# Kernel tuning notes

Hardware: AMD Instinct MI355X
Metric: run time of the kernel (lower is better)

The kernel has to match this reference:

```python
import jax, jax.numpy as jnp
from jax import lax
import numpy as np

C = 256       # residual_channels == skip_channels
B = 4
T = 4096
LATENT = 128
NB = 4        # n_blocks
NL = 10       # n_layers
ENC_DILS = tuple(2 ** i for i in range(NL)) * NB   # 40 encoder blocks
DEC_DILS = tuple(2 ** i for i in range(NL))        # 10 decoder blocks


def causal_conv(x, W, b, d):
    # x: [B, Cin, T], W: [Cout, Cin, k], left-pad by (k-1)*d for causality
    pad = (W.shape[-1] - 1) * d
    y = lax.conv_general_dilated(x, W, (1,), [(pad, 0)], rhs_dilation=(d,),
                                 dimension_numbers=('NCH', 'OIH', 'NCH'))
    return y + b[None, :, None]


def gated_block(h, Wf, bf, Wg, bg, Wr, br, Ws, bs, d):
    f = jnp.tanh(causal_conv(h, Wf, bf, d))
    g = jax.nn.sigmoid(causal_conv(h, Wg, bg, d))
    out = f * g
    res = jnp.einsum('oc,bct->bot', Wr, out) + br[None, :, None] + h
    skip = jnp.einsum('oc,bct->bot', Ws, out) + bs[None, :, None]
    return res, skip


def setup_inputs() -> dict:
    key = jax.random.key(0)
    ks = jax.random.split(key, 24)
    s = 0.05
    nE = NB * NL
    d = {}
    d['x'] = jax.random.normal(ks[0], (B, 1, T), jnp.float32)
    d['eps'] = jax.random.normal(ks[1], (B, LATENT), jnp.float32)
    d['enc_in_W'] = jax.random.normal(ks[2], (C, 1, 2)) * s
    d['enc_in_b'] = jnp.zeros((C,), jnp.float32)
    d['enc_Wf'] = jax.random.normal(ks[3], (nE, C, C, 2)) * s
    d['enc_bf'] = jnp.zeros((nE, C), jnp.float32)
    d['enc_Wg'] = jax.random.normal(ks[4], (nE, C, C, 2)) * s
    d['enc_bg'] = jnp.zeros((nE, C), jnp.float32)
    d['enc_Wr'] = jax.random.normal(ks[5], (nE, C, C)) * s
    d['enc_br'] = jnp.zeros((nE, C), jnp.float32)
    d['enc_Ws'] = jax.random.normal(ks[6], (nE, C, C)) * s
    d['enc_bs'] = jnp.zeros((nE, C), jnp.float32)
    d['fc_mu_W'] = jax.random.normal(ks[7], (LATENT, C)) * s
    d['fc_mu_b'] = jnp.zeros((LATENT,), jnp.float32)
    d['fc_lv_W'] = jax.random.normal(ks[8], (LATENT, C)) * s
    d['fc_lv_b'] = jnp.zeros((LATENT,), jnp.float32)
    d['dec_in_W'] = jax.random.normal(ks[9], (C, LATENT)) * s
    d['dec_in_b'] = jnp.zeros((C,), jnp.float32)
    d['dec_Wf'] = jax.random.normal(ks[10], (NL, C, C, 2)) * s
    d['dec_bf'] = jnp.zeros((NL, C), jnp.float32)
    d['dec_Wg'] = jax.random.normal(ks[11], (NL, C, C, 2)) * s
    d['dec_bg'] = jnp.zeros((NL, C), jnp.float32)
    d['dec_Wr'] = jax.random.normal(ks[12], (NL, C, C)) * s
    d['dec_br'] = jnp.zeros((NL, C), jnp.float32)
    d['out_W'] = jax.random.normal(ks[13], (1, C)) * s
    d['out_b'] = jnp.zeros((1,), jnp.float32)
    return d


def _forward(x, eps, enc_in_W, enc_in_b, enc_Wf, enc_bf, enc_Wg, enc_bg,
             enc_Wr, enc_br, enc_Ws, enc_bs, fc_mu_W, fc_mu_b, fc_lv_W, fc_lv_b,
             dec_in_W, dec_in_b, dec_Wf, dec_bf, dec_Wg, dec_bg, dec_Wr, dec_br,
             out_W, out_b):
    # --- encode ---
    h = causal_conv(x, enc_in_W, enc_in_b, 1)
    skip_sum = jnp.zeros((h.shape[0], C, h.shape[2]), h.dtype)
    for i, dil in enumerate(ENC_DILS):
        h, skip = gated_block(h, enc_Wf[i], enc_bf[i], enc_Wg[i], enc_bg[i],
                              enc_Wr[i], enc_br[i], enc_Ws[i], enc_bs[i], dil)
        skip_sum = skip_sum + skip
    pooled = skip_sum.mean(axis=-1)                      # [B, C]
    mu = pooled @ fc_mu_W.T + fc_mu_b                    # [B, LATENT]
    logvar = pooled @ fc_lv_W.T + fc_lv_b
    # --- reparameterize ---
    z = mu + eps * jnp.exp(0.5 * logvar)
    # --- decode (length-1 sequence) ---
    h2 = (jnp.einsum('ol,bl->bo', dec_in_W, z) + dec_in_b)[:, :, None]  # [B, C, 1]
    for i, dil in enumerate(DEC_DILS):
        f = jnp.tanh(causal_conv(h2, dec_Wf[i], dec_bf[i], dil))
        g = jax.nn.sigmoid(causal_conv(h2, dec_Wg[i], dec_bg[i], dil))
        out = f * g
        h2 = jnp.einsum('oc,bct->bot', dec_Wr[i], out) + dec_br[i][None, :, None] + h2
    y = jnp.einsum('oc,bct->bot', out_W, h2) + out_b[None, :, None]     # [B, 1, 1]
    return (y, mu, logvar)


def reference(x, eps, enc_in_W, enc_in_b, enc_Wf, enc_bf, enc_Wg, enc_bg,
              enc_Wr, enc_br, enc_Ws, enc_bs, fc_mu_W, fc_mu_b, fc_lv_W, fc_lv_b,
              dec_in_W, dec_in_b, dec_Wf, dec_bf, dec_Wg, dec_bg, dec_Wr, dec_br,
              out_W, out_b):
    return _forward(x, eps, enc_in_W, enc_in_b, enc_Wf, enc_bf, enc_Wg, enc_bg,
                    enc_Wr, enc_br, enc_Ws, enc_bs, fc_mu_W, fc_mu_b, fc_lv_W, fc_lv_b,
                    dec_in_W, dec_in_b, dec_Wf, dec_bf, dec_Wg, dec_bg, dec_Wr, dec_br,
                    out_W, out_b)
```

## Files before the change

kernel.cpp:

```cpp
#include <hip/hip_runtime.h>

typedef unsigned short u16;
typedef __attribute__((ext_vector_type(8))) __bf16 bf16x8;
typedef __attribute__((ext_vector_type(4))) float f32x4;

constexpr int C = 256;
constexpr int T = 4096;
constexpr int B = 4;
constexpr int NENC = 40;
constexpr int NDEC = 10;
constexpr int TILE = 64;

__device__ __forceinline__ float bf2f(u16 v) {
  union { unsigned u; float f; } x;
  x.u = ((unsigned)v) << 16;
  return x.f;
}
__device__ __forceinline__ u16 f2bf(float f) {
  union { float ff; unsigned u; } x;
  x.ff = f;
  unsigned r = x.u + 0x7fffu + ((x.u >> 16) & 1u);
  return (u16)(r >> 16);
}
__device__ __forceinline__ int swz(int row, int col) {
  int g = ((row & 7) ^ (row >> 3)) & 7;
  return row * 512 + (col ^ (g << 3));
}

typedef __attribute__((address_space(1))) const unsigned int* gp1_t;
typedef __attribute__((address_space(3))) unsigned int* lp3_t;
__device__ __forceinline__ void gl_lds16(const u16* g, u16* l) {
  __builtin_amdgcn_global_load_lds((gp1_t)(const void*)g, (lp3_t)(void*)l, 16, 0, 0);
}

__global__ void k_pack1(const float* __restrict__ Wf, const float* __restrict__ Wg,
                        u16* __restrict__ penc1, int total) {
  int p = blockIdx.x * 256 + threadIdx.x;
  if (p >= total) return;
  int lane = p & 63;
  int s = (p >> 6) & 3;
  int c = (p >> 8) & 15;
  int wv = (p >> 12) & 7;
  int layer = p >> 15;
  int co = wv * 32 + (s & 1) * 16 + (lane & 15);
  int k = c * 32 + (lane >> 4) * 8;
  const float* src = (s >= 2 ? Wg : Wf) + ((size_t)layer * C + co) * 512 + k;
  u16* dst = penc1 + (size_t)p * 8;
#pragma unroll
  for (int r = 0; r < 8; ++r) dst[r] = f2bf(src[r]);
}

__global__ void k_pack2(const float* __restrict__ Wr, u16* __restrict__ penc2, int total) {
  int p = blockIdx.x * 256 + threadIdx.x;
  if (p >= total) return;
  int lane = p & 63;
  int s = (p >> 6) & 1;
  int c = (p >> 7) & 7;
  int wv = (p >> 10) & 7;
  int layer = p >> 13;
  int co = wv * 32 + s * 16 + (lane & 15);
  int k = c * 32 + (lane >> 4) * 8;
  const float* src = Wr + ((size_t)layer * C + co) * 256 + k;
  u16* dst = penc2 + (size_t)p * 8;
#pragma unroll
  for (int r = 0; r < 8; ++r) dst[r] = f2bf(src[r]);
}

__global__ void k_packd(const float* __restrict__ dWf, const float* __restrict__ dWg,
                        const float* __restrict__ dWr, const float* __restrict__ dinW,
                        u16* __restrict__ pdfg, u16* __restrict__ pdr,
                        u16* __restrict__ tdin) {
  int p = blockIdx.x * 256 + threadIdx.x;
  if (p < 163840) {
    int lane = p & 63;
    int s = (p >> 6) & 1;
    int c = (p >> 7) & 7;
    int wv = (p >> 10) & 15;
    int layer = p >> 14;
    int co = wv * 16 + (lane & 15);
    int k = c * 32 + (lane >> 4) * 8;
    const float* src = (s ? dWg : dWf) + (((size_t)(layer * C + co)) * C + k) * 2 + 1;
    u16* dst = pdfg + (size_t)p * 8;
#pragma unroll
    for (int r = 0; r < 8; ++r) dst[r] = f2bf(src[2 * r]);
  } else if (p < 245760) {
    int q = p - 163840;
    int lane = q & 63;
    int c = (q >> 6) & 7;
    int wv = (q >> 9) & 15;
    int layer = q >> 13;
    int co = wv * 16 + (lane & 15);
    int k = c * 32 + (lane >> 4) * 8;
    const float* src = dWr + ((size_t)(layer * C + co)) * C + k;
    u16* dst = pdr + (size_t)q * 8;
#pragma unroll
    for (int r = 0; r < 8; ++r) dst[r] = f2bf(src[r]);
  } else if (p < 249856) {
    int u = p - 245760;
#pragma unroll
    for (int r = 0; r < 8; ++r) tdin[u * 8 + r] = f2bf(dinW[u * 8 + r]);
  }
}

__global__ void k_zero(float* __restrict__ p, int n) {
  int i = blockIdx.x * 256 + threadIdx.x;
  if (i < n) p[i] = 0.f;
}

__global__ void k_input(const float* __restrict__ x, const float* __restrict__ W,
                        const float* __restrict__ bin, float* __restrict__ h) {
  int idx = blockIdx.x * 256 + threadIdx.x;
  int t = idx & (T - 1);
  int c = (idx >> 12) & (C - 1);
  int b = idx >> 20;
  float xv = x[b * T + t];
  float xp = (t > 0) ? x[b * T + t - 1] : 0.f;
  h[idx] = W[2 * c] * xp + W[2 * c + 1] * xv + bin[c];
}

__global__ __launch_bounds__(512, 2) void k_enc(
    const float* __restrict__ hin, float* __restrict__ hout, float* __restrict__ rowsum_l,
    const u16* __restrict__ pw1, const float* __restrict__ bfb,
    const float* __restrict__ bgb,
    const u16* __restrict__ pw2, const float* __restrict__ brb,
    int dil) {
  extern __shared__ __align__(16) u16 smem[];
  u16* wb = smem + 64 * 512;
  const int tid = threadIdx.x;
  const int wave = tid >> 6;
  const int lane = tid & 63;
  const int ncol = lane & 15;
  const int quad = lane >> 4;
  const int wg = blockIdx.x;
  const int b = wg >> 6;
  const int t0 = (wg & 63) * TILE;
  const float* hb = hin + b * C * T;

  const int co0 = wave * 32;
  const int kq = quad * 8;
  const int off1 = (wg >> 3) & 15;
  const int off2 = (wg >> 3) & 7;
  const u16* b1 = pw1 + wave * 32768 + lane * 8;
  const u16* b2 = pw2 + wave * 8192 + lane * 8;
  u16* wreg0 = wb + wave * 2048;
  u16* wreg1 = wb + 16384 + wave * 2048;
  const int aoff = lane * 8;

#pragma unroll
  for (int cc = 0; cc < 2; ++cc) {
    u16* ld = cc ? wreg1 : wreg0;
    const u16* gs = b1 + ((off1 + cc) & 15) * 2048;
    gl_lds16(gs, ld);
    gl_lds16(gs + 512, ld + 512);
    gl_lds16(gs + 1024, ld + 1024);
    gl_lds16(gs + 1536, ld + 1536);
  }

  const int n4 = tid & 15;
  const int cib = tid >> 4;
  float4 v[16];
  const bool al4 = ((dil & 3) == 0);
  if (t0 >= dil) {
#pragma unroll
    for (int it2 = 0; it2 < 16; ++it2) {
      int ci = (cib + it2 * 32) & 255;
      int tap = it2 >> 3;
      int tb = t0 + n4 * 4 - (tap ? 0 : dil);
      const float* p = hb + ci * T + tb;
      if (tap || al4) {
        v[it2] = *(const float4*)p;
      } else {
        v[it2].x = p[0]; v[it2].y = p[1]; v[it2].z = p[2]; v[it2].w = p[3];
      }
    }
  } else {
#pragma unroll
    for (int it2 = 0; it2 < 16; ++it2) {
      int ci = (cib + it2 * 32) & 255;
      int tap = it2 >> 3;
      int tb = t0 + n4 * 4 - (tap ? 0 : dil);
      const float* p = hb + ci * T + tb;
      if (tap) {
        v[it2] = *(const float4*)p;
      } else {
        v[it2].x = (tb + 0 >= 0) ? p[0] : 0.f;
        v[it2].y = (tb + 1 >= 0) ? p[1] : 0.f;
        v[it2].z = (tb + 2 >= 0) ? p[2] : 0.f;
        v[it2].w = (tb + 3 >= 0) ? p[3] : 0.f;
      }
    }
  }
#pragma unroll
  for (int it2 = 0; it2 < 8; ++it2) {
    int ci = (cib + it2 * 32) & 255;
    const float* p0 = (const float*)&v[it2];
    const float* p1 = (const float*)&v[it2 + 8];
#pragma unroll
    for (int r = 0; r < 4; ++r) {
      unsigned w32 = (unsigned)f2bf(p0[r]) | ((unsigned)f2bf(p1[r]) << 16);
      *(unsigned*)(&smem[swz(n4 * 4 + r, 2 * ci)]) = w32;
    }
  }
  __syncthreads();

  f32x4 acc[4][4];
#pragma unroll
  for (int m = 0; m < 4; ++m)
#pragma unroll
    for (int nt = 0; nt < 4; ++nt)
      acc[m][nt] = (f32x4){0.f, 0.f, 0.f, 0.f};

#pragma unroll
  for (int c = 0; c < 16; ++c) {
    if (c < 15) asm volatile("s_waitcnt vmcnt(4)" ::: "memory");
    else        asm volatile("s_waitcnt vmcnt(0)" ::: "memory");
    const u16* wr_ = (c & 1) ? wreg1 : wreg0;
    bf16x8 af0 = *(const bf16x8*)(wr_ + aoff);
    bf16x8 af1 = *(const bf16x8*)(wr_ + 512 + aoff);
    bf16x8 af2 = *(const bf16x8*)(wr_ + 1024 + aoff);
    bf16x8 af3 = *(const bf16x8*)(wr_ + 1536 + aoff);
    const int kk = ((c + off1) & 15) * 32 + kq;
    bf16x8 bfr[4];
#pragma unroll
    for (int nt = 0; nt < 4; ++nt)
      bfr[nt] = *(const bf16x8*)(&smem[swz(nt * 16 + ncol, kk)]);
#pragma unroll
    for (int nt = 0; nt < 4; ++nt) {
      acc[0][nt] = __builtin_amdgcn_mfma_f32_16x16x32_bf16(af0, bfr[nt], acc[0][nt], 0, 0, 0);
      acc[1][nt] = __builtin_amdgcn_mfma_f32_16x16x32_bf16(af1, bfr[nt], acc[1][nt], 0, 0, 0);
      acc[2][nt] = __builtin_amdgcn_mfma_f32_16x16x32_bf16(af2, bfr[nt], acc[2][nt], 0, 0, 0);
      acc[3][nt] = __builtin_amdgcn_mfma_f32_16x16x32_bf16(af3, bfr[nt], acc[3][nt], 0, 0, 0);
    }
    if (c + 2 < 16) {
      asm volatile("s_waitcnt lgkmcnt(0)" ::: "memory");
      u16* ld = (c & 1) ? wreg1 : wreg0;
      const u16* gs = b1 + ((c + 2 + off1) & 15) * 2048;
      gl_lds16(gs, ld);
      gl_lds16(gs + 512, ld + 512);
      gl_lds16(gs + 1024, ld + 1024);
      gl_lds16(gs + 1536, ld + 1536);
    }
  }

#pragma unroll
  for (int cc = 0; cc < 2; ++cc) {
    u16* ld = cc ? wreg1 : wreg0;
    const u16* gs = b2 + ((off2 + cc) & 7) * 1024;
    gl_lds16(gs, ld);
    gl_lds16(gs + 512, ld + 512);
  }
  __syncthreads();

  float* rsb = rowsum_l + b * C;
#pragma unroll
  for (int j = 0; j < 2; ++j) {
    const int cob = co0 + j * 16 + quad * 4;
    float bfv[4], bgv[4], rs[4];
#pragma unroll
    for (int r = 0; r < 4; ++r) {
      bfv[r] = bfb[cob + r];
      bgv[r] = bgb[cob + r];
      rs[r] = 0.f;
    }
#pragma unroll
    for (int nt = 0; nt < 4; ++nt) {
      const int n = nt * 16 + ncol;
      u16 pk[4];
#pragma unroll
      for (int r = 0; r < 4; ++r) {
        float fv = acc[j][nt][r] + bfv[r];
        float gv = acc[2 + j][nt][r] + bgv[r];
        float th = 1.f - 2.f / (__expf(2.f * fv) + 1.f);
        float sg = 1.f / (1.f + __expf(-gv));
        float o = th * sg;
        rs[r] += o;
        pk[r] = f2bf(o);
      }
      uint2 w;
      w.x = (unsigned)pk[0] | ((unsigned)pk[1] << 16);
      w.y = (unsigned)pk[2] | ((unsigned)pk[3] << 16);
      *(uint2*)(&smem[swz(n, cob)]) = w;
    }
#pragma unroll
    for (int r = 0; r < 4; ++r) {
      float s = rs[r];
      s += __shfl_xor(s, 1);
      s += __shfl_xor(s, 2);
      s += __shfl_xor(s, 4);
      s += __shfl_xor(s, 8);
      if (ncol == 0) atomicAdd(&rsb[cob + r], s);
    }
  }
  __syncthreads();

  f32x4 acc2[2][4];
#pragma unroll
  for (int m = 0; m < 2; ++m)
#pragma unroll
    for (int nt = 0; nt < 4; ++nt)
      acc2[m][nt] = (f32x4){0.f, 0.f, 0.f, 0.f};

#pragma unroll
  for (int c = 0; c < 8; ++c) {
    if (c < 7) asm volatile("s_waitcnt vmcnt(2)" ::: "memory");
    else       asm volatile("s_waitcnt vmcnt(0)" ::: "memory");
    const u16* wr_ = (c & 1) ? wreg1 : wreg0;
    bf16x8 af0 = *(const bf16x8*)(wr_ + aoff);
    bf16x8 af1 = *(const bf16x8*)(wr_ + 512 + aoff);
    const int kk = ((c + off2) & 7) * 32 + kq;
    bf16x8 bfr[4];
#pragma unroll
    for (int nt = 0; nt < 4; ++nt)
      bfr[nt] = *(const bf16x8*)(&smem[swz(nt * 16 + ncol, kk)]);
#pragma unroll
    for (int nt = 0; nt < 4; ++nt) {
      acc2[0][nt] = __builtin_amdgcn_mfma_f32_16x16x32_bf16(af0, bfr[nt], acc2[0][nt], 0, 0, 0);
      acc2[1][nt] = __builtin_amdgcn_mfma_f32_16x16x32_bf16(af1, bfr[nt], acc2[1][nt], 0, 0, 0);
    }
    if (c + 2 < 8) {
      asm volatile("s_waitcnt lgkmcnt(0)" ::: "memory");
      u16* ld = (c & 1) ? wreg1 : wreg0;
      const u16* gs = b2 + ((c + 2 + off2) & 7) * 1024;
      gl_lds16(gs, ld);
      gl_lds16(gs + 512, ld + 512);
    }
  }
  __syncthreads();

  float* fb = (float*)smem;
#pragma unroll
  for (int m = 0; m < 2; ++m) {
    const int cob = co0 + m * 16 + quad * 4;
#pragma unroll
    for (int nt = 0; nt < 4; ++nt) {
      const int t = nt * 16 + ncol;
#pragma unroll
      for (int r = 0; r < 4; ++r)
        fb[(cob + r) * 66 + t] = acc2[m][nt][r] + brb[cob + r];
    }
  }
  __syncthreads();
  float* ho = hout + b * C * T;
#pragma unroll
  for (int it2 = 0; it2 < 8; ++it2) {
    const int ci = cib + it2 * 32;
    const float* fr = fb + ci * 66 + n4 * 4;
    float4 o;
    o.x = fr[0] + v[it2 + 8].x;
    o.y = fr[1] + v[it2 + 8].y;
    o.z = fr[2] + v[it2 + 8].z;
    o.w = fr[3] + v[it2 + 8].w;
    *(float4*)(ho + ci * T + t0 + n4 * 4) = o;
  }
}

__global__ __launch_bounds__(256) void k_skip(
    const float* __restrict__ encWs, const float* __restrict__ encbs,
    const float* __restrict__ rowsum, float* __restrict__ pooled) {
  __shared__ float rs[B][C];
  const int l = blockIdx.x;
  const int co = threadIdx.x;
  for (int i = co; i < B * C; i += 256) rs[i >> 8][i & 255] = rowsum[l * B * C + i];
  __syncthreads();
  const float* Wrow = encWs + (size_t)l * C * C + co * C;
  float bs = encbs[l * C + co] * (float)T;
  float d[B] = {0.f, 0.f, 0.f, 0.f};
  for (int ci = 0; ci < C; ci += 4) {
    float4 w = *(const float4*)(Wrow + ci);
#pragma unroll
    for (int b = 0; b < B; ++b)
      d[b] += w.x * rs[b][ci] + w.y * rs[b][ci + 1] + w.z * rs[b][ci + 2] + w.w * rs[b][ci + 3];
  }
#pragma unroll
  for (int b = 0; b < B; ++b) atomicAdd(&pooled[b * C + co], d[b] + bs);
}

__global__ __launch_bounds__(256) void k_fc(
    const float* __restrict__ pooled,
    const float* __restrict__ muW, const float* __restrict__ mub,
    const float* __restrict__ lvW, const float* __restrict__ lvb,
    float* __restrict__ mlbuf, float* __restrict__ dout) {
  __shared__ float pm[B * C];
  const int tid = threadIdx.x;
  for (int i = tid; i < B * C; i += 256) pm[i] = pooled[i] * (1.f / (float)T);
  __syncthreads();
  const int waveG = blockIdx.x * 4 + (tid >> 6);
  const int lane = tid & 63;
  for (int j = 0; j < 16; ++j) {
    int d = waveG * 16 + j;
    int b = d >> 8, r = d & 255, which = r >> 7, l = r & 127;
    const float* Wrow = (which ? lvW : muW) + l * C;
    const float* p = pm + b * C;
    float s = Wrow[lane] * p[lane] + Wrow[lane + 64] * p[lane + 64] +
              Wrow[lane + 128] * p[lane + 128] + Wrow[lane + 192] * p[lane + 192];
#pragma unroll
    for (int off = 32; off; off >>= 1) s += __shfl_xor(s, off);
    if (lane == 0) {
      float val = s + (which ? lvb[l] : mub[l]);
      mlbuf[which * 512 + b * 128 + l] = val;
      dout[4 + which * 512 + b * 128 + l] = val;
    }
  }
}

__global__ __launch_bounds__(1024, 1) void k_dec(
    const float* __restrict__ mlbuf, const float* __restrict__ eps,
    const u16* __restrict__ tdin, const float* __restrict__ dinb,
    const u16* __restrict__ pdfg, const float* __restrict__ dbf,
    const float* __restrict__ dbg,
    const u16* __restrict__ pdr, const float* __restrict__ dbr,
    const float* __restrict__ outW, const float* __restrict__ outb,
    float* __restrict__ dout) {
  extern __shared__ __align__(16) u16 dsm[];
  __shared__ __align__(16) u16 Ah[16][264];
  __shared__ __align__(16) u16 Ao[16][264];
  __shared__ float h2f[4][256];
  __shared__ float outred[4];
  const int tid = threadIdx.x;
  const int wave = tid >> 6;
  const int lane = tid & 63;
  const int ncol = lane & 15;
  const int quad = lane >> 4;
  const int kq = quad * 8;
  const int co = wave * 16 + ncol;
  u16* wreg = dsm + wave * 4096;

  bf16x8 tdw[4];
  {
    const u16* wp = tdin + co * 128;
#pragma unroll
    for (int it = 0; it < 4; ++it) tdw[it] = *(const bf16x8*)(wp + it * 32 + kq);
  }

  if (tid < 512) {
    int b = tid >> 7, l = tid & 127;
    float mu = mlbuf[b * 128 + l];
    float lv = mlbuf[512 + b * 128 + l];
    Ah[b][l] = f2bf(mu + eps[b * 128 + l] * expf(0.5f * lv));
  }
  if (tid < 4) outred[tid] = 0.f;
  __syncthreads();

  {
    f32x4 acch = (f32x4){0.f, 0.f, 0.f, 0.f};
#pragma unroll
    for (int it = 0; it < 4; ++it) {
      bf16x8 af = *(const bf16x8*)(&Ah[ncol][it * 32 + kq]);
      acch = __builtin_amdgcn_mfma_f32_16x16x32_bf16(af, tdw[it], acch, 0, 0, 0);
    }
    __syncthreads();
    if (quad == 0) {
      float bias = dinb[co];
#pragma unroll
      for (int r = 0; r < 4; ++r) {
        float hv = acch[r] + bias;
        h2f[r][co] = hv;
        Ah[r][co] = f2bf(hv);
      }
    }
  }
  {
    const u16* fb = pdfg + wave * 8192 + lane * 8;
#pragma unroll
    for (int cc = 0; cc < 4; ++cc) {
      gl_lds16(fb + cc * 1024, wreg + cc * 1024);
      gl_lds16(fb + cc * 1024 + 512, wreg + cc * 1024 + 512);
    }
  }
  __syncthreads();

  for (int i = 0; i < NDEC; ++i) {
    const u16* fb = pdfg + (i * 16 + wave) * 8192 + lane * 8;
    const u16* rb = pdr + (i * 16 + wave) * 4096 + lane * 8;

    f32x4 accf = (f32x4){0.f, 0.f, 0.f, 0.f};
    f32x4 accg = (f32x4){0.f, 0.f, 0.f, 0.f};
#pragma unroll
    for (int c = 0; c < 8; ++c) {
      if (c == 4) asm volatile("s_waitcnt vmcnt(6)" ::: "memory");
      else if (c == 5) asm volatile("s_waitcnt vmcnt(4)" ::: "memory");
      else if (c == 6) asm volatile("s_waitcnt vmcnt(2)" ::: "memory");
      else if (c == 7) asm volatile("s_waitcnt vmcnt(0)" ::: "memory");
      const u16* bufp = wreg + (c & 3) * 1024;
      bf16x8 bf_ = *(const bf16x8*)(bufp + lane * 8);
      bf16x8 bg_ = *(const bf16x8*)(bufp + 512 + lane * 8);
      bf16x8 af = *(const bf16x8*)(&Ah[ncol][c * 32 + kq]);
      accf = __builtin_amdgcn_mfma_f32_16x16x32_bf16(af, bf_, accf, 0, 0, 0);
      accg = __builtin_amdgcn_mfma_f32_16x16x32_bf16(af, bg_, accg, 0, 0, 0);
      if (c < 4) {
        asm volatile("s_waitcnt lgkmcnt(0)" ::: "memory");
        gl_lds16(fb + (c + 4) * 1024, wreg + (c & 3) * 1024);
        gl_lds16(fb + (c + 4) * 1024 + 512, wreg + (c & 3) * 1024 + 512);
      }
    }
    asm volatile("s_waitcnt lgkmcnt(0)" ::: "memory");
#pragma unroll
    for (int cc = 0; cc < 4; ++cc) gl_lds16(rb + cc * 512, wreg + cc * 1024);

    if (quad == 0) {
      float bfv = dbf[i * C + co];
      float bgv = dbg[i * C + co];
#pragma unroll
      for (int r = 0; r < 4; ++r) {
        float fv = accf[r] + bfv;
        float gv = accg[r] + bgv;
        float th = 1.f - 2.f / (__expf(2.f * fv) + 1.f);
        float sg = 1.f / (1.f + __expf(-gv));
        Ao[r][co] = f2bf(th * sg);
      }
    }
    __syncthreads();

    f32x4 accr = (f32x4){0.f, 0.f, 0.f, 0.f};
#pragma unroll
    for (int c = 0; c < 8; ++c) {
      if (c == 4) asm volatile("s_waitcnt vmcnt(3)" ::: "memory");
      else if (c == 5) asm volatile("s_waitcnt vmcnt(2)" ::: "memory");
      else if (c == 6) asm volatile("s_waitcnt vmcnt(1)" ::: "memory");
      else if (c == 7) asm volatile("s_waitcnt vmcnt(0)" ::: "memory");
      bf16x8 br_ = *(const bf16x8*)(wreg + (c & 3) * 1024 + lane * 8);
      bf16x8 af = *(const bf16x8*)(&Ao[ncol][c * 32 + kq]);
      accr = __builtin_amdgcn_mfma_f32_16x16x32_bf16(af, br_, accr, 0, 0, 0);
      if (c < 4) {
        asm volatile("s_waitcnt lgkmcnt(0)" ::: "memory");
        gl_lds16(rb + (c + 4) * 512, wreg + (c & 3) * 1024);
      }
    }
    if (i + 1 < NDEC) {
      const u16* nfb = pdfg + ((i + 1) * 16 + wave) * 8192 + lane * 8;
      asm volatile("s_waitcnt lgkmcnt(0)" ::: "memory");
#pragma unroll
      for (int cc = 0; cc < 4; ++cc) {
        gl_lds16(nfb + cc * 1024, wreg + cc * 1024);
        gl_lds16(nfb + cc * 1024 + 512, wreg + cc * 1024 + 512);
      }
    }
    if (quad == 0) {
      float brv = dbr[i * C + co];
#pragma unroll
      for (int r = 0; r < 4; ++r) {
        float hv = h2f[r][co] + accr[r] + brv;
        h2f[r][co] = hv;
        Ah[r][co] = f2bf(hv);
      }
    }
    __syncthreads();
  }

  {
    int b = tid >> 8, c = tid & 255;
    float val = outW[c] * h2f[b][c];
#pragma unroll
    for (int off = 32; off; off >>= 1) val += __shfl_xor(val, off);
    if (lane == 0) atomicAdd(&outred[b], val);
  }
  __syncthreads();
  if (tid < 4) dout[tid] = outred[tid] + outb[0];
}

extern "C" void kernel_launch(void* const* d_in, const int* in_sizes, int n_in,
                              void* d_out, int out_size, void* d_ws, size_t ws_size,
                              hipStream_t stream) {
  const float* x      = (const float*)d_in[0];
  const float* eps    = (const float*)d_in[1];
  const float* encinW = (const float*)d_in[2];
  const float* encinb = (const float*)d_in[3];
  const float* encWf  = (const float*)d_in[4];
  const float* encbf  = (const float*)d_in[5];
  const float* encWg  = (const float*)d_in[6];
  const float* encbg  = (const float*)d_in[7];
  const float* encWr  = (const float*)d_in[8];
  const float* encbr  = (const float*)d_in[9];
  const float* encWs  = (const float*)d_in[10];
  const float* encbs  = (const float*)d_in[11];
  const float* muW    = (const float*)d_in[12];
  const float* mub    = (const float*)d_in[13];
  const float* lvW    = (const float*)d_in[14];
  const float* lvb    = (const float*)d_in[15];
  const float* dinW   = (const float*)d_in[16];
  const float* dinb   = (const float*)d_in[17];
  const float* dWf    = (const float*)d_in[18];
  const float* dbf    = (const float*)d_in[19];
  const float* dWg    = (const float*)d_in[20];
  const float* dbg    = (const float*)d_in[21];
  const float* dWr    = (const float*)d_in[22];
  const float* dbr    = (const float*)d_in[23];
  const float* outW   = (const float*)d_in[24];
  const float* outb   = (const float*)d_in[25];
  float* dout = (float*)d_out;

  char* ws = (char*)d_ws;
  float* hA = (float*)ws;
  float* hB = hA + (size_t)B * C * T;
  float* pooled = hB + (size_t)B * C * T;
  float* mlbuf = pooled + B * C;
  float* rowsum = mlbuf + 1024;
  u16* penc1 = (u16*)(rowsum + NENC * B * C);
  u16* penc2 = penc1 + (size_t)10485760;
  u16* pdfg = penc2 + (size_t)2621440;
  u16* pdr = pdfg + (size_t)1310720;
  u16* tdin = pdr + (size_t)655360;

  (void)hipFuncSetAttribute(reinterpret_cast<const void*>(k_enc),
                            hipFuncAttributeMaxDynamicSharedMemorySize, 131072);
  (void)hipFuncSetAttribute(reinterpret_cast<const void*>(k_dec),
                            hipFuncAttributeMaxDynamicSharedMemorySize, 131072);

  k_pack1<<<(1310720 + 255) / 256, 256, 0, stream>>>(encWf, encWg, penc1, 1310720);
  k_pack2<<<(327680 + 255) / 256, 256, 0, stream>>>(encWr, penc2, 327680);
  k_packd<<<(249856 + 255) / 256, 256, 0, stream>>>(dWf, dWg, dWr, dinW, pdfg, pdr, tdin);

  const int nZ = B * C + 1024 + NENC * B * C;
  k_zero<<<(nZ + 255) / 256, 256, 0, stream>>>(pooled, nZ);
  k_input<<<(B * C * T) / 256, 256, 0, stream>>>(x, encinW, encinb, hA);

  for (int i = 0; i < NENC; ++i) {
    const int dil = 1 << (i % 10);
    const float* hi = (i & 1) ? hB : hA;
    float* ho = (i & 1) ? hA : hB;
    k_enc<<<256, 512, 131072, stream>>>(
        hi, ho, rowsum + (size_t)i * B * C,
        penc1 + (size_t)i * 262144, encbf + (size_t)i * C,
        encbg + (size_t)i * C,
        penc2 + (size_t)i * 65536, encbr + (size_t)i * C,
        dil);
  }

  k_skip<<<NENC, 256, 0, stream>>>(encWs, encbs, rowsum, pooled);
  k_fc<<<16, 256, 0, stream>>>(pooled, muW, mub, lvW, lvb, mlbuf, dout);
  k_dec<<<1, 1024, 131072, stream>>>(mlbuf, eps, tdin, dinb, pdfg, dbf, dbg,
                                     pdr, dbr, outW, outb, dout);
}
```

Baseline: 1.287 ms.

## Fuse 40 encoder launches into a persistent kernel with per-tile dataflow flags

The 40 per-layer encoder launches become one persistent kernel that loops over layers inside each workgroup. Per-(layer, batch, tile) flags in workspace replace kernel boundaries. Before reading its input, a workgroup spins until the previous layer's needed neighbouring tiles, including those that still read the buffer it will overwrite, have published their results. This removes launch gaps and whole-grid barriers between layers so fast tiles can move ahead. The cost is spin-wait overhead, and it depends on all 256 workgroups being resident at once.

```diff
diff --git a/kernel.cpp b/kernel.cpp
--- a/kernel.cpp
+++ b/kernel.cpp
@@ -118,12 +118,12 @@
   h[idx] = W[2 * c] * xp + W[2 * c + 1] * xv + bin[c];
 }
 
-__global__ __launch_bounds__(512, 2) void k_enc(
-    const float* __restrict__ hin, float* __restrict__ hout, float* __restrict__ rowsum_l,
-    const u16* __restrict__ pw1, const float* __restrict__ bfb,
-    const float* __restrict__ bgb,
-    const u16* __restrict__ pw2, const float* __restrict__ brb,
-    int dil) {
+__global__ __launch_bounds__(512, 2) void k_encp(
+    float* __restrict__ hA, float* __restrict__ hB, float* __restrict__ rowsum,
+    const u16* __restrict__ penc1, const float* __restrict__ encbf,
+    const float* __restrict__ encbg,
+    const u16* __restrict__ penc2, const float* __restrict__ encbr,
+    int* __restrict__ flags) {
   extern __shared__ __align__(16) u16 smem[];
   u16* wb = smem + 64 * 512;
   const int tid = threadIdx.x;
@@ -133,224 +133,258 @@
   const int quad = lane >> 4;
   const int wg = blockIdx.x;
   const int b = wg >> 6;
-  const int t0 = (wg & 63) * TILE;
-  const float* hb = hin + b * C * T;
+  const int tile = wg & 63;
+  const int t0 = tile * TILE;
 
   const int co0 = wave * 32;
   const int kq = quad * 8;
   const int off1 = (wg >> 3) & 15;
   const int off2 = (wg >> 3) & 7;
-  const u16* b1 = pw1 + wave * 32768 + lane * 8;
-  const u16* b2 = pw2 + wave * 8192 + lane * 8;
+  const int n4 = tid & 15;
+  const int cib = tid >> 4;
+  const int aoff = lane * 8;
   u16* wreg0 = wb + wave * 2048;
   u16* wreg1 = wb + 16384 + wave * 2048;
-  const int aoff = lane * 8;
-
-#pragma unroll
-  for (int cc = 0; cc < 2; ++cc) {
-    u16* ld = cc ? wreg1 : wreg0;
-    const u16* gs = b1 + ((off1 + cc) & 15) * 2048;
-    gl_lds16(gs, ld);
-    gl_lds16(gs + 512, ld + 512);
-    gl_lds16(gs + 1024, ld + 1024);
-    gl_lds16(gs + 1536, ld + 1536);
-  }
-
-  const int n4 = tid & 15;
-  const int cib = tid >> 4;
-  float4 v[16];
-  const bool al4 = ((dil & 3) == 0);
-  if (t0 >= dil) {
-#pragma unroll
-    for (int it2 = 0; it2 < 16; ++it2) {
-      int ci = (cib + it2 * 32) & 255;
-      int tap = it2 >> 3;
-      int tb = t0 + n4 * 4 - (tap ? 0 : dil);
-      const float* p = hb + ci * T + tb;
-      if (tap || al4) {
-        v[it2] = *(const float4*)p;
-      } else {
-        v[it2].x = p[0]; v[it2].y = p[1]; v[it2].z = p[2]; v[it2].w = p[3];
-      }
-    }
-  } else {
-#pragma unroll
-    for (int it2 = 0; it2 < 16; ++it2) {
-      int ci = (cib + it2 * 32) & 255;
-      int tap = it2 >> 3;
-      int tb = t0 + n4 * 4 - (tap ? 0 : dil);
-      const float* p = hb + ci * T + tb;
-      if (tap) {
-        v[it2] = *(const float4*)p;
-      } else {
-        v[it2].x = (tb + 0 >= 0) ? p[0] : 0.f;
-        v[it2].y = (tb + 1 >= 0) ? p[1] : 0.f;
-        v[it2].z = (tb + 2 >= 0) ? p[2] : 0.f;
-        v[it2].w = (tb + 3 >= 0) ? p[3] : 0.f;
-      }
-    }
-  }
-#pragma unroll
-  for (int it2 = 0; it2 < 8; ++it2) {
-    int ci = (cib + it2 * 32) & 255;
-    const float* p0 = (const float*)&v[it2];
-    const float* p1 = (const float*)&v[it2 + 8];
-#pragma unroll
-    for (int r = 0; r < 4; ++r) {
-      unsigned w32 = (unsigned)f2bf(p0[r]) | ((unsigned)f2bf(p1[r]) << 16);
-      *(unsigned*)(&smem[swz(n4 * 4 + r, 2 * ci)]) = w32;
-    }
-  }
-  __syncthreads();
-
-  f32x4 acc[4][4];
-#pragma unroll
-  for (int m = 0; m < 4; ++m)
-#pragma unroll
-    for (int nt = 0; nt < 4; ++nt)
-      acc[m][nt] = (f32x4){0.f, 0.f, 0.f, 0.f};
-
-#pragma unroll
-  for (int c = 0; c < 16; ++c) {
-    if (c < 15) asm volatile("s_waitcnt vmcnt(4)" ::: "memory");
-    else        asm volatile("s_waitcnt vmcnt(0)" ::: "memory");
-    const u16* wr_ = (c & 1) ? wreg1 : wreg0;
-    bf16x8 af0 = *(const bf16x8*)(wr_ + aoff);
-    bf16x8 af1 = *(const bf16x8*)(wr_ + 512 + aoff);
-    bf16x8 af2 = *(const bf16x8*)(wr_ + 1024 + aoff);
-    bf16x8 af3 = *(const bf16x8*)(wr_ + 1536 + aoff);
-    const int kk = ((c + off1) & 15) * 32 + kq;
-    bf16x8 bfr[4];
-#pragma unroll
-    for (int nt = 0; nt < 4; ++nt)
-      bfr[nt] = *(const bf16x8*)(&smem[swz(nt * 16 + ncol, kk)]);
-#pragma unroll
-    for (int nt = 0; nt < 4; ++nt) {
-      acc[0][nt] = __builtin_amdgcn_mfma_f32_16x16x32_bf16(af0, bfr[nt], acc[0][nt], 0, 0, 0);
-      acc[1][nt] = __builtin_amdgcn_mfma_f32_16x16x32_bf16(af1, bfr[nt], acc[1][nt], 0, 0, 0);
-      acc[2][nt] = __builtin_amdgcn_mfma_f32_16x16x32_bf16(af2, bfr[nt], acc[2][nt], 0, 0, 0);
-      acc[3][nt] = __builtin_amdgcn_mfma_f32_16x16x32_bf16(af3, bfr[nt], acc[3][nt], 0, 0, 0);
-    }
-    if (c + 2 < 16) {
-      asm volatile("s_waitcnt lgkmcnt(0)" ::: "memory");
-      u16* ld = (c & 1) ? wreg1 : wreg0;
-      const u16* gs = b1 + ((c + 2 + off1) & 15) * 2048;
+
+  for (int i = 0; i < NENC; ++i) {
+    const int dil = 1 << (i % 10);
+    const float* hi = (i & 1) ? hB : hA;
+    float* ho = (i & 1) ? hA : hB;
+    const float* hb = hi + b * C * T;
+    const u16* b1 = penc1 + (size_t)i * 262144 + wave * 32768 + lane * 8;
+    const u16* b2 = penc2 + (size_t)i * 65536 + wave * 8192 + lane * 8;
+    const float* bfb = encbf + i * C;
+    const float* bgb = encbg + i * C;
+    const float* brb = encbr + i * C;
+
+#pragma unroll
+    for (int cc = 0; cc < 2; ++cc) {
+      u16* ld = cc ? wreg1 : wreg0;
+      const u16* gs = b1 + ((off1 + cc) & 15) * 2048;
       gl_lds16(gs, ld);
       gl_lds16(gs + 512, ld + 512);
       gl_lds16(gs + 1024, ld + 1024);
       gl_lds16(gs + 1536, ld + 1536);
     }
-  }
-
-#pragma unroll
-  for (int cc = 0; cc < 2; ++cc) {
-    u16* ld = cc ? wreg1 : wreg0;
-    const u16* gs = b2 + ((off2 + cc) & 7) * 1024;
-    gl_lds16(gs, ld);
-    gl_lds16(gs + 512, ld + 512);
-  }
-  __syncthreads();
-
-  float* rsb = rowsum_l + b * C;
-#pragma unroll
-  for (int j = 0; j < 2; ++j) {
-    const int cob = co0 + j * 16 + quad * 4;
-    float bfv[4], bgv[4], rs[4];
-#pragma unroll
-    for (int r = 0; r < 4; ++r) {
-      bfv[r] = bfb[cob + r];
-      bgv[r] = bgb[cob + r];
-      rs[r] = 0.f;
-    }
-#pragma unroll
-    for (int nt = 0; nt < 4; ++nt) {
-      const int n = nt * 16 + ncol;
-      u16 pk[4];
+
+    if (i > 0) {
+      const int dprev = 1 << ((i - 1) % 10);
+      int lo = t0 - dil;
+      lo = (lo < 0) ? 0 : (lo >> 6);
+      int hiT = tile + ((dprev + 63) >> 6);
+      if (hiT > 63) hiT = 63;
+      if (wave == 0) {
+        const int n = hiT - lo + 1;
+        if (lane < n) {
+          const int* fp = flags + ((i - 1) * 4 + b) * 64 + lo + lane;
+          while (__hip_atomic_load(fp, __ATOMIC_ACQUIRE, __HIP_MEMORY_SCOPE_AGENT) == 0)
+            __builtin_amdgcn_s_sleep(2);
+        }
+      }
+      __syncthreads();
+    }
+
+    float4 v[16];
+    const bool al4 = ((dil & 3) == 0);
+    if (t0 >= dil) {
+#pragma unroll
+      for (int it2 = 0; it2 < 16; ++it2) {
+        int ci = (cib + it2 * 32) & 255;
+        int tap = it2 >> 3;
+        int tb = t0 + n4 * 4 - (tap ? 0 : dil);
+        const float* p = hb + ci * T + tb;
+        if (tap || al4) {
+          v[it2] = *(const float4*)p;
+        } else {
+          v[it2].x = p[0]; v[it2].y = p[1]; v[it2].z = p[2]; v[it2].w = p[3];
+        }
+      }
+    } else {
+#pragma unroll
+      for (int it2 = 0; it2 < 16; ++it2) {
+        int ci = (cib + it2 * 32) & 255;
+        int tap = it2 >> 3;
+        int tb = t0 + n4 * 4 - (tap ? 0 : dil);
+        const float* p = hb + ci * T + tb;
+        if (tap) {
+          v[it2] = *(const float4*)p;
+        } else {
+          v[it2].x = (tb + 0 >= 0) ? p[0] : 0.f;
+          v[it2].y = (tb + 1 >= 0) ? p[1] : 0.f;
+          v[it2].z = (tb + 2 >= 0) ? p[2] : 0.f;
+          v[it2].w = (tb + 3 >= 0) ? p[3] : 0.f;
+        }
+      }
+    }
+#pragma unroll
+    for (int it2 = 0; it2 < 8; ++it2) {
+      int ci = (cib + it2 * 32) & 255;
+      const float* p0 = (const float*)&v[it2];
+      const float* p1 = (const float*)&v[it2 + 8];
 #pragma unroll
       for (int r = 0; r < 4; ++r) {
-        float fv = acc[j][nt][r] + bfv[r];
-        float gv = acc[2 + j][nt][r] + bgv[r];
-        float th = 1.f - 2.f / (__expf(2.f * fv) + 1.f);
-        float sg = 1.f / (1.f + __expf(-gv));
-        float o = th * sg;
-        rs[r] += o;
-        pk[r] = f2bf(o);
-      }
-      uint2 w;
-      w.x = (unsigned)pk[0] | ((unsigned)pk[1] << 16);
-      w.y = (unsigned)pk[2] | ((unsigned)pk[3] << 16);
-      *(uint2*)(&smem[swz(n, cob)]) = w;
-    }
-#pragma unroll
-    for (int r = 0; r < 4; ++r) {
-      float s = rs[r];
-      s += __shfl_xor(s, 1);
-      s += __shfl_xor(s, 2);
-      s += __shfl_xor(s, 4);
-      s += __shfl_xor(s, 8);
-      if (ncol == 0) atomicAdd(&rsb[cob + r], s);
-    }
-  }
-  __syncthreads();
-
-  f32x4 acc2[2][4];
-#pragma unroll
-  for (int m = 0; m < 2; ++m)
-#pragma unroll
-    for (int nt = 0; nt < 4; ++nt)
-      acc2[m][nt] = (f32x4){0.f, 0.f, 0.f, 0.f};
-
-#pragma unroll
-  for (int c = 0; c < 8; ++c) {
-    if (c < 7) asm volatile("s_waitcnt vmcnt(2)" ::: "memory");
-    else       asm volatile("s_waitcnt vmcnt(0)" ::: "memory");
-    const u16* wr_ = (c & 1) ? wreg1 : wreg0;
-    bf16x8 af0 = *(const bf16x8*)(wr_ + aoff);
-    bf16x8 af1 = *(const bf16x8*)(wr_ + 512 + aoff);
-    const int kk = ((c + off2) & 7) * 32 + kq;
-    bf16x8 bfr[4];
-#pragma unroll
-    for (int nt = 0; nt < 4; ++nt)
-      bfr[nt] = *(const bf16x8*)(&smem[swz(nt * 16 + ncol, kk)]);
-#pragma unroll
-    for (int nt = 0; nt < 4; ++nt) {
-      acc2[0][nt] = __builtin_amdgcn_mfma_f32_16x16x32_bf16(af0, bfr[nt], acc2[0][nt], 0, 0, 0);
-      acc2[1][nt] = __builtin_amdgcn_mfma_f32_16x16x32_bf16(af1, bfr[nt], acc2[1][nt], 0, 0, 0);
-    }
-    if (c + 2 < 8) {
-      asm volatile("s_waitcnt lgkmcnt(0)" ::: "memory");
-      u16* ld = (c & 1) ? wreg1 : wreg0;
-      const u16* gs = b2 + ((c + 2 + off2) & 7) * 1024;
+        unsigned w32 = (unsigned)f2bf(p0[r]) | ((unsigned)f2bf(p1[r]) << 16);
+        *(unsigned*)(&smem[swz(n4 * 4 + r, 2 * ci)]) = w32;
+      }
+    }
+    __syncthreads();
+
+    f32x4 acc[4][4];
+#pragma unroll
+    for (int m = 0; m < 4; ++m)
+#pragma unroll
+      for (int nt = 0; nt < 4; ++nt)
+        acc[m][nt] = (f32x4){0.f, 0.f, 0.f, 0.f};
+
+#pragma unroll
+    for (int c = 0; c < 16; ++c) {
+      if (c < 15) asm volatile("s_waitcnt vmcnt(4)" ::: "memory");
+      else        asm volatile("s_waitcnt vmcnt(0)" ::: "memory");
+      const u16* wr_ = (c & 1) ? wreg1 : wreg0;
+      bf16x8 af0 = *(const bf16x8*)(wr_ + aoff);
+      bf16x8 af1 = *(const bf16x8*)(wr_ + 512 + aoff);
+      bf16x8 af2 = *(const bf16x8*)(wr_ + 1024 + aoff);
+      bf16x8 af3 = *(const bf16x8*)(wr_ + 1536 + aoff);
+      const int kk = ((c + off1) & 15) * 32 + kq;
+      bf16x8 bfr[4];
+#pragma unroll
+      for (int nt = 0; nt < 4; ++nt)
+        bfr[nt] = *(const bf16x8*)(&smem[swz(nt * 16 + ncol, kk)]);
+#pragma unroll
+      for (int nt = 0; nt < 4; ++nt) {
+        acc[0][nt] = __builtin_amdgcn_mfma_f32_16x16x32_bf16(af0, bfr[nt], acc[0][nt], 0, 0, 0);
+        acc[1][nt] = __builtin_amdgcn_mfma_f32_16x16x32_bf16(af1, bfr[nt], acc[1][nt], 0, 0, 0);
+        acc[2][nt] = __builtin_amdgcn_mfma_f32_16x16x32_bf16(af2, bfr[nt], acc[2][nt], 0, 0, 0);
+        acc[3][nt] = __builtin_amdgcn_mfma_f32_16x16x32_bf16(af3, bfr[nt], acc[3][nt], 0, 0, 0);
+      }
+      if (c + 2 < 16) {
+        asm volatile("s_waitcnt lgkmcnt(0)" ::: "memory");
+        u16* ld = (c & 1) ? wreg1 : wreg0;
+        const u16* gs = b1 + ((c + 2 + off1) & 15) * 2048;
+        gl_lds16(gs, ld);
+        gl_lds16(gs + 512, ld + 512);
+        gl_lds16(gs + 1024, ld + 1024);
+        gl_lds16(gs + 1536, ld + 1536);
+      }
+    }
+
+#pragma unroll
+    for (int cc = 0; cc < 2; ++cc) {
+      u16* ld = cc ? wreg1 : wreg0;
+      const u16* gs = b2 + ((off2 + cc) & 7) * 1024;
       gl_lds16(gs, ld);
       gl_lds16(gs + 512, ld + 512);
     }
-  }
-  __syncthreads();
-
-  float* fb = (float*)smem;
-#pragma unroll
-  for (int m = 0; m < 2; ++m) {
-    const int cob = co0 + m * 16 + quad * 4;
-#pragma unroll
-    for (int nt = 0; nt < 4; ++nt) {
-      const int t = nt * 16 + ncol;
-#pragma unroll
-      for (int r = 0; r < 4; ++r)
-        fb[(cob + r) * 66 + t] = acc2[m][nt][r] + brb[cob + r];
-    }
-  }
-  __syncthreads();
-  float* ho = hout + b * C * T;
-#pragma unroll
-  for (int it2 = 0; it2 < 8; ++it2) {
-    const int ci = cib + it2 * 32;
-    const float* fr = fb + ci * 66 + n4 * 4;
-    float4 o;
-    o.x = fr[0] + v[it2 + 8].x;
-    o.y = fr[1] + v[it2 + 8].y;
-    o.z = fr[2] + v[it2 + 8].z;
-    o.w = fr[3] + v[it2 + 8].w;
-    *(float4*)(ho + ci * T + t0 + n4 * 4) = o;
+    __syncthreads();
+
+    float* rsb = rowsum + (size_t)i * B * C + b * C;
+#pragma unroll
+    for (int j = 0; j < 2; ++j) {
+      const int cob = co0 + j * 16 + quad * 4;
+      float bfv[4], bgv[4], rs[4];
+#pragma unroll
+      for (int r = 0; r < 4; ++r) {
+        bfv[r] = bfb[cob + r];
+        bgv[r] = bgb[cob + r];
+        rs[r] = 0.f;
+      }
+#pragma unroll
+      for (int nt = 0; nt < 4; ++nt) {
+        const int n = nt * 16 + ncol;
+        u16 pk[4];
+#pragma unroll
+        for (int r = 0; r < 4; ++r) {
+          float fv = acc[j][nt][r] + bfv[r];
+          float gv = acc[2 + j][nt][r] + bgv[r];
+          float th = 1.f - 2.f / (__expf(2.f * fv) + 1.f);
+          float sg = 1.f / (1.f + __expf(-gv));
+          float o = th * sg;
+          rs[r] += o;
+          pk[r] = f2bf(o);
+        }
+        uint2 w;
+        w.x = (unsigned)pk[0] | ((unsigned)pk[1] << 16);
+        w.y = (unsigned)pk[2] | ((unsigned)pk[3] << 16);
+        *(uint2*)(&smem[swz(n, cob)]) = w;
+      }
+#pragma unroll
+      for (int r = 0; r < 4; ++r) {
+        float s = rs[r];
+        s += __shfl_xor(s, 1);
+        s += __shfl_xor(s, 2);
+        s += __shfl_xor(s, 4);
+        s += __shfl_xor(s, 8);
+        if (ncol == 0) atomicAdd(&rsb[cob + r], s);
+      }
+    }
+    __syncthreads();
+
+    f32x4 acc2[2][4];
+#pragma unroll
+    for (int m = 0; m < 2; ++m)
+#pragma unroll
+      for (int nt = 0; nt < 4; ++nt)
+        acc2[m][nt] = (f32x4){0.f, 0.f, 0.f, 0.f};
+
+#pragma unroll
+    for (int c = 0; c < 8; ++c) {
+      if (c < 7) asm volatile("s_waitcnt vmcnt(2)" ::: "memory");
+      else       asm volatile("s_waitcnt vmcnt(0)" ::: "memory");
+      const u16* wr_ = (c & 1) ? wreg1 : wreg0;
+      bf16x8 af0 = *(const bf16x8*)(wr_ + aoff);
+      bf16x8 af1 = *(const bf16x8*)(wr_ + 512 + aoff);
+      const int kk = ((c + off2) & 7) * 32 + kq;
+      bf16x8 bfr[4];
+#pragma unroll
+      for (int nt = 0; nt < 4; ++nt)
+        bfr[nt] = *(const bf16x8*)(&smem[swz(nt * 16 + ncol, kk)]);
+#pragma unroll
+      for (int nt = 0; nt < 4; ++nt) {
+        acc2[0][nt] = __builtin_amdgcn_mfma_f32_16x16x32_bf16(af0, bfr[nt], acc2[0][nt], 0, 0, 0);
+        acc2[1][nt] = __builtin_amdgcn_mfma_f32_16x16x32_bf16(af1, bfr[nt], acc2[1][nt], 0, 0, 0);
+      }
+      if (c + 2 < 8) {
+        asm volatile("s_waitcnt lgkmcnt(0)" ::: "memory");
+        u16* ld = (c & 1) ? wreg1 : wreg0;
+        const u16* gs = b2 + ((c + 2 + off2) & 7) * 1024;
+        gl_lds16(gs, ld);
+        gl_lds16(gs + 512, ld + 512);
+      }
+    }
+    __syncthreads();
+
+    float* fb = (float*)smem;
+#pragma unroll
+    for (int m = 0; m < 2; ++m) {
+      const int cob = co0 + m * 16 + quad * 4;
+#pragma unroll
+      for (int nt = 0; nt < 4; ++nt) {
+        const int t = nt * 16 + ncol;
+#pragma unroll
+        for (int r = 0; r < 4; ++r)
+          fb[(cob + r) * 66 + t] = acc2[m][nt][r] + brb[cob + r];
+      }
+    }
+    __syncthreads();
+    float* ho2 = ho + b * C * T;
+#pragma unroll
+    for (int it2 = 0; it2 < 8; ++it2) {
+      const int ci = cib + it2 * 32;
+      const float* fr = fb + ci * 66 + n4 * 4;
+      float4 o;
+      o.x = fr[0] + v[it2 + 8].x;
+      o.y = fr[1] + v[it2 + 8].y;
+      o.z = fr[2] + v[it2 + 8].z;
+      o.w = fr[3] + v[it2 + 8].w;
+      *(float4*)(ho2 + ci * T + t0 + n4 * 4) = o;
+    }
+
+    __syncthreads();
+    if (i + 1 < NENC && tid == 0) {
+      __threadfence();
+      __hip_atomic_fetch_add(&flags[(i * 4 + b) * 64 + tile], 1,
+                             __ATOMIC_RELEASE, __HIP_MEMORY_SCOPE_AGENT);
+    }
   }
 }
 
@@ -595,13 +629,14 @@
   float* pooled = hB + (size_t)B * C * T;
   float* mlbuf = pooled + B * C;
   float* rowsum = mlbuf + 1024;
-  u16* penc1 = (u16*)(rowsum + NENC * B * C);
+  int* flags = (int*)(rowsum + NENC * B * C);
+  u16* penc1 = (u16*)(flags + NENC * B * 64);
   u16* penc2 = penc1 + (size_t)10485760;
   u16* pdfg = penc2 + (size_t)2621440;
   u16* pdr = pdfg + (size_t)1310720;
   u16* tdin = pdr + (size_t)655360;
 
-  (void)hipFuncSetAttribute(reinterpret_cast<const void*>(k_enc),
+  (void)hipFuncSetAttribute(reinterpret_cast<const void*>(k_encp),
                             hipFuncAttributeMaxDynamicSharedMemorySize, 131072);
   (void)hipFuncSetAttribute(reinterpret_cast<const void*>(k_dec),
                             hipFuncAttributeMaxDynamicSharedMemorySize, 131072);
@@ -610,21 +645,12 @@
   k_pack2<<<(327680 + 255) / 256, 256, 0, stream>>>(encWr, penc2, 327680);
   k_packd<<<(249856 + 255) / 256, 256, 0, stream>>>(dWf, dWg, dWr, dinW, pdfg, pdr, tdin);
 
-  const int nZ = B * C + 1024 + NENC * B * C;
+  const int nZ = 1024 + 1024 + NENC * B * C + NENC * B * 64;
   k_zero<<<(nZ + 255) / 256, 256, 0, stream>>>(pooled, nZ);
   k_input<<<(B * C * T) / 256, 256, 0, stream>>>(x, encinW, encinb, hA);
 
-  for (int i = 0; i < NENC; ++i) {
-    const int dil = 1 << (i % 10);
-    const float* hi = (i & 1) ? hB : hA;
-    float* ho = (i & 1) ? hA : hB;
-    k_enc<<<256, 512, 131072, stream>>>(
-        hi, ho, rowsum + (size_t)i * B * C,
-        penc1 + (size_t)i * 262144, encbf + (size_t)i * C,
-        encbg + (size_t)i * C,
-        penc2 + (size_t)i * 65536, encbr + (size_t)i * C,
-        dil);
-  }
+  k_encp<<<256, 512, 131072, stream>>>(hA, hB, rowsum, penc1, encbf, encbg,
+                                       penc2, encbr, flags);
 
   k_skip<<<NENC, 256, 0, stream>>>(encWs, encbs, rowsum, pooled);
   k_fc<<<16, 256, 0, stream>>>(pooled, muW, mub, lvW, lvb, mlbuf, dout);
```

New measurement: 2.416 ms. 1.88x slower.
